# Kernel optimization log

Hardware: AMD Instinct MI355X
Metric: run time of the kernel (lower is better)

## Reference

```python
import jax, jax.numpy as jnp
import numpy as np

HEADS = 8
DIM_HEAD = 64
SCALE = DIM_HEAD ** -0.5


def setup_inputs() -> dict:
    key = jax.random.key(0)
    k1, k2, k3 = jax.random.split(key, 3)
    B, N, D = 4, 2048, HEADS * DIM_HEAD  # D = inner_dim = 512
    x = jax.random.normal(k1, (B, N, D), dtype=jnp.float32)
    # nn.Linear weights stored transposed vs torch; here we use [in, out]
    w_qkv = jax.random.normal(k2, (D, 3 * D), dtype=jnp.float32) * (D ** -0.5)
    w_out = jax.random.normal(k3, (D, D), dtype=jnp.float32) * (D ** -0.5)
    b_out = jnp.zeros((D,), dtype=jnp.float32)
    return {"x": x, "w_qkv": w_qkv, "w_out": w_out, "b_out": b_out}


def reference(x, w_qkv, w_out, b_out):
    B, N, D = x.shape
    qkv = x @ w_qkv  # [B, N, 3D]
    q, k, v = jnp.split(qkv, 3, axis=-1)

    def to_heads(t):  # b n (h d) -> b h n d
        return t.reshape(B, N, HEADS, DIM_HEAD).transpose(0, 2, 1, 3)

    q, k, v = to_heads(q), to_heads(k), to_heads(v)
    dots = jnp.einsum('bhnd,bhmd->bhnm', q, k) * SCALE  # [B,H,N,N]
    attn = jax.nn.softmax(dots, axis=-1)
    out = jnp.einsum('bhnm,bhmd->bhnd', attn, v)  # [B,H,N,d]
    out = out.transpose(0, 2, 1, 3).reshape(B, N, D)  # b h n d -> b n (h d)
    return out @ w_out + b_out
```

## Files before the change

### kernel.cpp

```cpp
#include <hip/hip_runtime.h>

typedef __bf16 bf16;
typedef __bf16 bf16x8 __attribute__((ext_vector_type(8)));
typedef __bf16 bf16x4 __attribute__((ext_vector_type(4)));
typedef float f32x4 __attribute__((ext_vector_type(4)));
typedef float f32x16 __attribute__((ext_vector_type(16)));
typedef unsigned int uint2v __attribute__((ext_vector_type(2)));

#define MFMA16(a, b, c) __builtin_amdgcn_mfma_f32_16x16x32_bf16(a, b, c, 0, 0, 0)
#define MFMA32(a, b, c) __builtin_amdgcn_mfma_f32_32x32x16_bf16(a, b, c, 0, 0, 0)

#define CS 0.18033688011112042f

#if __has_builtin(__builtin_amdgcn_exp2f)
#define EXP2(x) __builtin_amdgcn_exp2f(x)
#else
#define EXP2(x) exp2f(x)
#endif

#define WAIT_VM0() __builtin_amdgcn_s_waitcnt(0x0F70)
#define WAIT_VM6() __builtin_amdgcn_s_waitcnt(0x0F76)
#define WAIT_VM8() __builtin_amdgcn_s_waitcnt(0x0F78)

#define BARRIER() __builtin_amdgcn_s_barrier()
#define CFENCE() asm volatile("" ::: "memory")

__device__ __forceinline__ void load_lds16(const bf16* g, bf16* l) {
    __builtin_amdgcn_global_load_lds(
        (const __attribute__((address_space(1))) unsigned int*)g,
        (__attribute__((address_space(3))) unsigned int*)l, 16, 0, 0);
}

#if __has_builtin(__builtin_amdgcn_permlane32_swap)
__device__ __forceinline__ bf16x8 build_bfrag(bf16x4 plo, bf16x4 phi, int ) {
    union { bf16x4 b; unsigned int i[2]; } ul, uh;
    ul.b = plo; uh.b = phi;
    uint2v r0 = __builtin_amdgcn_permlane32_swap(ul.i[0], uh.i[0], false, false);
    uint2v r1 = __builtin_amdgcn_permlane32_swap(ul.i[1], uh.i[1], false, false);
    union { unsigned int i[4]; bf16x8 b; } ub;
    ub.i[0] = r0[0]; ub.i[1] = r1[0]; ub.i[2] = r0[1]; ub.i[3] = r1[1];
    return ub.b;
}

__device__ __forceinline__ float sum_halves(float x) {
    union { float f; unsigned int u; } a; a.f = x;
    uint2v r = __builtin_amdgcn_permlane32_swap(a.u, a.u, false, false);
    union { unsigned int u; float f; } b0, b1;
    b0.u = r[0]; b1.u = r[1];
    return b0.f + b1.f;
}
#else
__device__ __forceinline__ bf16x4 shfl_xor32_b64(bf16x4 v) {
    union { bf16x4 b; int i[2]; } u;
    u.b = v;
    u.i[0] = __shfl_xor(u.i[0], 32, 64);
    u.i[1] = __shfl_xor(u.i[1], 32, 64);
    return u.b;
}
__device__ __forceinline__ bf16x8 build_bfrag(bf16x4 plo, bf16x4 phi, int h) {
    bf16x4 xlo = shfl_xor32_b64(plo);
    bf16x4 xhi = shfl_xor32_b64(phi);
    bf16x4 lo4 = h ? xhi : plo;
    bf16x4 hi4 = h ? phi : xlo;
    bf16x8 bb;
#pragma unroll
    for (int i = 0; i < 4; ++i) { bb[i] = lo4[i]; bb[4 + i] = hi4[i]; }
    return bb;
}
__device__ __forceinline__ float sum_halves(float x) {
    return x + __shfl_xor(x, 32, 64);
}
#endif

__global__ __launch_bounds__(256) void prep_kernel(const float* __restrict__ x,
                                                   const float* __restrict__ w_qkv,
                                                   const float* __restrict__ w_out,
                                                   bf16* __restrict__ xb,
                                                   bf16* __restrict__ wqkvT,
                                                   bf16* __restrict__ woutT) {
    __shared__ float tile[32][33];
    int bid = blockIdx.x, t = threadIdx.x;
    if (bid < 4096) {
        int i = (bid * 256 + t) * 4;
        float4 v = *(const float4*)&x[i];
        bf16x4 o = {(bf16)v.x, (bf16)v.y, (bf16)v.z, (bf16)v.w};
        *(bf16x4*)&xb[i] = o;
        return;
    }
    const float* in; bf16* out; int C, bx, by;
    if (bid < 4864) { int b2 = bid - 4096; in = w_qkv; out = wqkvT; C = 1536; bx = b2 % 48; by = b2 / 48; }
    else            { int b3 = bid - 4864; in = w_out; out = woutT; C = 512;  bx = b3 & 15; by = b3 >> 4; }
    const int R = 512;
    int tx = t & 31, ty = t >> 5;
    int c0 = bx * 32, r0 = by * 32;
#pragma unroll
    for (int i = ty; i < 32; i += 8)
        tile[i][tx] = in[(size_t)(r0 + i) * C + c0 + tx];
    __syncthreads();
#pragma unroll
    for (int i = ty; i < 32; i += 8)
        out[(size_t)(c0 + i) * R + r0 + tx] = (bf16)tile[tx][i];
}

__global__ __launch_bounds__(256) void transpose_v_kernel(const bf16* __restrict__ qkv,
                                                          bf16* __restrict__ vt) {
    __shared__ bf16 tile[64][68];
    int t = threadIdx.x;
    int bh = blockIdx.z, b = bh >> 3, hd = bh & 7;
    int n0 = blockIdx.x * 64;
    int rr = t >> 4, c4 = (t & 15) * 4;
#pragma unroll
    for (int p = 0; p < 4; ++p) {
        int r = p * 16 + rr;
        *(bf16x4*)&tile[r][c4] =
            *(const bf16x4*)&qkv[(size_t)(b * 2048 + n0 + r) * 1536 + 1024 + hd * 64 + c4];
    }
    __syncthreads();
#pragma unroll
    for (int p = 0; p < 4; ++p) {
        int d = p * 16 + rr;
        bf16x4 o = {tile[c4][d], tile[c4 + 1][d], tile[c4 + 2][d], tile[c4 + 3][d]};
        *(bf16x4*)&vt[(size_t)(bh * 64 + d) * 2048 + n0 + c4] = o;
    }
}

template <int MT, int MODE, typename OutT>
__global__ __launch_bounds__(256, (MT == 4) ? 2 : 3)
void gemm_bt_kernel(const bf16* __restrict__ A,
                    const bf16* __restrict__ Bt,
                    const float* __restrict__ bias,
                    OutT* __restrict__ C,
                    int M, int N, int K) {
    const int BM = MT * 32;
    const int ASZ = BM * 64, BSZ = 128 * 64;
    __shared__ bf16 As[2 * ASZ];
    __shared__ bf16 Bs[2 * BSZ];
    int t = threadIdx.x;
    int lane = t & 63, w = t >> 6;
    int wr = w >> 1, wc = w & 1;
    int quad = lane >> 4, r16 = lane & 15;

    int lin = blockIdx.y * gridDim.x + blockIdx.x;
    int cpx = (gridDim.x * gridDim.y) >> 3;
    int nl = (lin & 7) * cpx + (lin >> 3);
    int bx = nl % gridDim.x, by = nl / gridDim.x;
    int m0 = by * BM, n0 = bx * 128;

    const f32x4 fzero = {0.f, 0.f, 0.f, 0.f};
    f32x4 acc[MT][4];
#pragma unroll
    for (int i = 0; i < MT; ++i)
#pragma unroll
        for (int j = 0; j < 4; ++j) acc[i][j] = fzero;

    const bf16* ap[MT]; bf16* ad[MT];
    const bf16* bp[4];  bf16* bd[4];
#pragma unroll
    for (int i = 0; i < MT; ++i) {
        int ci = i * 256 + t;
        int row = ci >> 3, cp = ci & 7, cc = cp ^ (row & 7);
        ap[i] = &A[(size_t)(m0 + row) * K + cc * 8];
        ad[i] = &As[ci * 8];
    }
#pragma unroll
    for (int i = 0; i < 4; ++i) {
        int ci = i * 256 + t;
        int row = ci >> 3, cp = ci & 7, cc = cp ^ (row & 7);
        bp[i] = &Bt[(size_t)(n0 + row) * K + cc * 8];
        bd[i] = &Bs[ci * 8];
    }

    auto stage = [&](int par) {
#pragma unroll
        for (int i = 0; i < MT; ++i) { load_lds16(ap[i], ad[i] + par * ASZ); ap[i] += 64; }
#pragma unroll
        for (int i = 0; i < 4; ++i) { load_lds16(bp[i], bd[i] + par * BSZ); bp[i] += 64; }
    };

    stage(0);
    int nk = K >> 6;
    for (int kk = 0; kk < nk; ++kk) {
        if (kk + 1 < nk) {
            stage((kk + 1) & 1);
            if constexpr (MT == 4) WAIT_VM8(); else WAIT_VM6();
        } else {
            WAIT_VM0();
        }
        CFENCE(); BARRIER(); CFENCE();

        const bf16* Asb = &As[(kk & 1) * ASZ];
        const bf16* Bsb = &Bs[(kk & 1) * BSZ];
#pragma unroll
        for (int ks = 0; ks < 2; ++ks) {
            bf16x8 af[MT], bfr[4];
            int cp = (ks * 4 + quad) ^ (r16 & 7);
#pragma unroll
            for (int mt = 0; mt < MT; ++mt)
                af[mt] = *(const bf16x8*)&Asb[(wr * (BM / 2) + mt * 16 + r16) * 64 + cp * 8];
#pragma unroll
            for (int nt = 0; nt < 4; ++nt)
                bfr[nt] = *(const bf16x8*)&Bsb[(wc * 64 + nt * 16 + r16) * 64 + cp * 8];
#pragma unroll
            for (int mt = 0; mt < MT; ++mt)
#pragma unroll
                for (int nt = 0; nt < 4; ++nt)
                    acc[mt][nt] = MFMA16(af[mt], bfr[nt], acc[mt][nt]);
        }
        if (kk + 1 < nk) { CFENCE(); BARRIER(); CFENCE(); }
    }
#pragma unroll
    for (int mt = 0; mt < MT; ++mt)
#pragma unroll
        for (int nt = 0; nt < 4; ++nt)
#pragma unroll
            for (int r = 0; r < 4; ++r) {
                int row = m0 + wr * (BM / 2) + mt * 16 + quad * 4 + r;
                int col = n0 + wc * 64 + nt * 16 + r16;
                float v = acc[mt][nt][r];
                if (MODE == 1 && n0 < 512) v *= CS;
                if (MODE == 2) v += bias[col];
                C[(size_t)row * N + col] = (OutT)v;
            }
}

__global__ __launch_bounds__(128, 2) void attn_kernel(const bf16* __restrict__ qkv,
                                                      const bf16* __restrict__ vt,
                                                      bf16* __restrict__ out) {
    __shared__ __align__(16) char smemraw[32768];
    bf16* stage = (bf16*)smemraw;

    int t = threadIdx.x;
    int lane = t & 63, w = t >> 6;
    int h = lane >> 5, q = lane & 31;
    int bh = blockIdx.y, b = bh >> 3, hd = bh & 7;
    int qb = blockIdx.x * 64;

    bf16x8 qf[2][4];
#pragma unroll
    for (int sub = 0; sub < 2; ++sub) {
        size_t qoff = (size_t)(b * 2048 + qb + sub * 32 + q) * 1536 + hd * 64;
#pragma unroll
        for (int s = 0; s < 4; ++s)
            qf[sub][s] = *(const bf16x8*)&qkv[qoff + s * 16 + h * 8];
    }

    f32x16 o_acc[2][2];
#pragma unroll
    for (int sub = 0; sub < 2; ++sub)
#pragma unroll
        for (int db = 0; db < 2; ++db)
#pragma unroll
            for (int i = 0; i < 16; ++i) o_acc[sub][db][i] = 0.f;
    float psum[2] = {0.f, 0.f};

    bf16* base = stage + w * 8192;

    const bf16* kp[4]; const bf16* vp[4];
    int kdo[4], vdo[4];
#pragma unroll
    for (int rdd = 0; rdd < 4; ++rdd) {
        int ciK = rdd * 64 + lane;
        int rowK = ciK >> 3, ccK = (ciK & 7) ^ (rowK & 7);
        kp[rdd] = &qkv[(size_t)(b * 2048 + w * 1024 + rowK) * 1536 + 512 + hd * 64 + ccK * 8];
        kdo[rdd] = ciK * 8;
        int ciV = rdd * 64 + lane;
        int rowV = ciV >> 2, ccV = (ciV & 3) ^ (rowV & 3);
        vp[rdd] = &vt[(size_t)(bh * 64 + rowV) * 2048 + w * 1024 + ccV * 8];
        vdo[rdd] = 2048 + ciV * 8;
    }

#pragma unroll
    for (int rdd = 0; rdd < 4; ++rdd) {
        load_lds16(kp[rdd], base + kdo[rdd]);  kp[rdd] += (size_t)32 * 1536;
        load_lds16(vp[rdd], base + vdo[rdd]);  vp[rdd] += 32;
    }

    for (int it = 0; it < 32; ++it) {
        const bf16* Ks = base + (it & 1) * 4096;
        const bf16* Vs = Ks + 2048;
        if (it < 31) {
            bf16* nb = base + ((it + 1) & 1) * 4096;
#pragma unroll
            for (int rdd = 0; rdd < 4; ++rdd) {
                load_lds16(kp[rdd], nb + kdo[rdd]);  kp[rdd] += (size_t)32 * 1536;
                load_lds16(vp[rdd], nb + vdo[rdd]);  vp[rdd] += 32;
            }
            WAIT_VM8();
        } else {
            WAIT_VM0();
        }

        bf16x8 kf[4];
#pragma unroll
        for (int s = 0; s < 4; ++s) {
            int cp = (s * 2 + h) ^ (q & 7);
            kf[s] = *(const bf16x8*)&Ks[q * 64 + cp * 8];
        }
        bf16x8 vf[2][2];
#pragma unroll
        for (int kstep = 0; kstep < 2; ++kstep)
#pragma unroll
            for (int db = 0; db < 2; ++db) {
                int cp = (kstep * 2 + h) ^ (q & 3);
                vf[kstep][db] = *(const bf16x8*)&Vs[(db * 32 + q) * 32 + cp * 8];
            }

#pragma unroll
        for (int sub = 0; sub < 2; ++sub) {
            f32x16 sacc;
#pragma unroll
            for (int i = 0; i < 16; ++i) sacc[i] = 0.f;
#pragma unroll
            for (int s = 0; s < 4; ++s)
                sacc = MFMA32(kf[s], qf[sub][s], sacc);

            bf16x4 pk[4];
            float ps0 = 0.f, ps1 = 0.f, ps2 = 0.f, ps3 = 0.f;
#pragma unroll
            for (int i = 0; i < 4; ++i) {
                float p0 = EXP2(sacc[i]);
                float p1 = EXP2(sacc[4 + i]);
                float p2 = EXP2(sacc[8 + i]);
                float p3 = EXP2(sacc[12 + i]);
                ps0 += p0; ps1 += p1; ps2 += p2; ps3 += p3;
                pk[0][i] = (bf16)p0; pk[1][i] = (bf16)p1;
                pk[2][i] = (bf16)p2; pk[3][i] = (bf16)p3;
            }
            psum[sub] += (ps0 + ps1) + (ps2 + ps3);
            bf16x8 bfr0 = build_bfrag(pk[0], pk[1], h);
            bf16x8 bfr1 = build_bfrag(pk[2], pk[3], h);

#pragma unroll
            for (int db = 0; db < 2; ++db) {
                o_acc[sub][db] = MFMA32(vf[0][db], bfr0, o_acc[sub][db]);
                o_acc[sub][db] = MFMA32(vf[1][db], bfr1, o_acc[sub][db]);
            }
        }
    }

    float l_own[2];
#pragma unroll
    for (int sub = 0; sub < 2; ++sub)
        l_own[sub] = sum_halves(psum[sub]);

    __syncthreads();
    float* Of = (float*)smemraw;
    float* Lf = (float*)(smemraw + 17408);

    if (w == 1) {
#pragma unroll
        for (int sub = 0; sub < 2; ++sub) {
#pragma unroll
            for (int db = 0; db < 2; ++db)
#pragma unroll
                for (int r = 0; r < 16; ++r) {
                    int d = db * 32 + (r & 3) + 8 * (r >> 2) + 4 * h;
                    Of[(sub * 32 + q) * 68 + d] = o_acc[sub][db][r];
                }
            if (h == 0) Lf[sub * 32 + q] = l_own[sub];
        }
    }
    __syncthreads();
    if (w == 0) {
#pragma unroll
        for (int sub = 0; sub < 2; ++sub) {
#pragma unroll
            for (int db = 0; db < 2; ++db)
#pragma unroll
                for (int r = 0; r < 16; ++r) {
                    int d = db * 32 + (r & 3) + 8 * (r >> 2) + 4 * h;
                    Of[(sub * 32 + q) * 68 + d] += o_acc[sub][db][r];
                }
            if (h == 0) Lf[sub * 32 + q] += l_own[sub];
        }
    }
    __syncthreads();

    {
        int row = t >> 1, half = t & 1;
        float linv = 1.f / Lf[row];
        const float* src = &Of[row * 68 + half * 32];
        bf16* dst = &out[(size_t)(b * 2048 + qb + row) * 512 + hd * 64 + half * 32];
#pragma unroll
        for (int i = 0; i < 4; ++i) {
            f32x4 a = *(const f32x4*)&src[i * 8];
            f32x4 c = *(const f32x4*)&src[i * 8 + 4];
            bf16x8 o8;
#pragma unroll
            for (int j = 0; j < 4; ++j) {
                o8[j] = (bf16)(a[j] * linv);
                o8[4 + j] = (bf16)(c[j] * linv);
            }
            *(bf16x8*)&dst[i * 8] = o8;
        }
    }
}

extern "C" void kernel_launch(void* const* d_in, const int* in_sizes, int n_in,
                              void* d_out, int out_size, void* d_ws, size_t ws_size,
                              hipStream_t stream) {
    const float* x     = (const float*)d_in[0];
    const float* w_qkv = (const float*)d_in[1];
    const float* w_out = (const float*)d_in[2];
    const float* b_out = (const float*)d_in[3];
    float* out = (float*)d_out;

    char* ws = (char*)d_ws;
    size_t off = 0;
    bf16* xb    = (bf16*)(ws + off); off += (size_t)8192 * 512 * 2;
    bf16* wqkvT = (bf16*)(ws + off); off += (size_t)1536 * 512 * 2;
    bf16* woutT = (bf16*)(ws + off); off += (size_t)512 * 512 * 2;
    bf16* qkv   = (bf16*)(ws + off); off += (size_t)8192 * 1536 * 2;
    bf16* vt    = (bf16*)(ws + off); off += (size_t)32 * 64 * 2048 * 2;
    bf16* attn  = (bf16*)(ws + off);

    prep_kernel<<<5120, 256, 0, stream>>>(x, w_qkv, w_out, xb, wqkvT, woutT);
    gemm_bt_kernel<4, 1, bf16><<<dim3(12, 64), 256, 0, stream>>>(
        xb, wqkvT, nullptr, qkv, 8192, 1536, 512);
    transpose_v_kernel<<<dim3(32, 1, 32), 256, 0, stream>>>(qkv, vt);
    attn_kernel<<<dim3(32, 32), 128, 0, stream>>>(qkv, vt, attn);
    gemm_bt_kernel<2, 2, float><<<dim3(4, 128), 256, 0, stream>>>(
        attn, woutT, b_out, out, 8192, 512, 512);
}
```

Measured before the change: 159.6 us.

## Split attention key range across four waves with staggered K/V pipelining

The attention kernel now runs four waves per block instead of two, each covering 512 keys, so the key range is split more finely within a block. Its load pipeline changes to double-buffer K while V uses a single buffer, and QK/softmax for one tile is interleaved with the V load and PV of the previous tile. The cross-wave reduction of partial outputs grows to four serialized LDS accumulation steps. This costs more LDS per block (48KB) and more barriers at the end, in exchange for more waves in flight to hide latency.

```diff
diff --git a/kernel.cpp b/kernel.cpp
--- a/kernel.cpp
+++ b/kernel.cpp
@@ -19,6 +19,7 @@
 #endif
 
 #define WAIT_VM0() __builtin_amdgcn_s_waitcnt(0x0F70)
+#define WAIT_VM4() __builtin_amdgcn_s_waitcnt(0x0F74)
 #define WAIT_VM6() __builtin_amdgcn_s_waitcnt(0x0F76)
 #define WAIT_VM8() __builtin_amdgcn_s_waitcnt(0x0F78)
 
@@ -223,10 +224,10 @@
             }
 }
 
-__global__ __launch_bounds__(128, 2) void attn_kernel(const bf16* __restrict__ qkv,
+__global__ __launch_bounds__(256, 3) void attn_kernel(const bf16* __restrict__ qkv,
                                                       const bf16* __restrict__ vt,
                                                       bf16* __restrict__ out) {
-    __shared__ __align__(16) char smemraw[32768];
+    __shared__ __align__(16) char smemraw[49152];
     bf16* stage = (bf16*)smemraw;
 
     int t = threadIdx.x;
@@ -253,7 +254,8 @@
             for (int i = 0; i < 16; ++i) o_acc[sub][db][i] = 0.f;
     float psum[2] = {0.f, 0.f};
 
-    bf16* base = stage + w * 8192;
+    bf16* base = stage + w * 6144;
+    bf16* Vs = base + 4096;
 
     const bf16* kp[4]; const bf16* vp[4];
     int kdo[4], vdo[4];
@@ -261,59 +263,39 @@
     for (int rdd = 0; rdd < 4; ++rdd) {
         int ciK = rdd * 64 + lane;
         int rowK = ciK >> 3, ccK = (ciK & 7) ^ (rowK & 7);
-        kp[rdd] = &qkv[(size_t)(b * 2048 + w * 1024 + rowK) * 1536 + 512 + hd * 64 + ccK * 8];
+        kp[rdd] = &qkv[(size_t)(b * 2048 + w * 512 + rowK) * 1536 + 512 + hd * 64 + ccK * 8];
         kdo[rdd] = ciK * 8;
         int ciV = rdd * 64 + lane;
         int rowV = ciV >> 2, ccV = (ciV & 3) ^ (rowV & 3);
-        vp[rdd] = &vt[(size_t)(bh * 64 + rowV) * 2048 + w * 1024 + ccV * 8];
-        vdo[rdd] = 2048 + ciV * 8;
-    }
-
-#pragma unroll
-    for (int rdd = 0; rdd < 4; ++rdd) {
-        load_lds16(kp[rdd], base + kdo[rdd]);  kp[rdd] += (size_t)32 * 1536;
-        load_lds16(vp[rdd], base + vdo[rdd]);  vp[rdd] += 32;
-    }
-
-    for (int it = 0; it < 32; ++it) {
-        const bf16* Ks = base + (it & 1) * 4096;
-        const bf16* Vs = Ks + 2048;
-        if (it < 31) {
-            bf16* nb = base + ((it + 1) & 1) * 4096;
-#pragma unroll
-            for (int rdd = 0; rdd < 4; ++rdd) {
-                load_lds16(kp[rdd], nb + kdo[rdd]);  kp[rdd] += (size_t)32 * 1536;
-                load_lds16(vp[rdd], nb + vdo[rdd]);  vp[rdd] += 32;
-            }
-            WAIT_VM8();
-        } else {
-            WAIT_VM0();
-        }
-
-        bf16x8 kf[4];
-#pragma unroll
-        for (int s = 0; s < 4; ++s) {
-            int cp = (s * 2 + h) ^ (q & 7);
-            kf[s] = *(const bf16x8*)&Ks[q * 64 + cp * 8];
-        }
-        bf16x8 vf[2][2];
-#pragma unroll
-        for (int kstep = 0; kstep < 2; ++kstep)
-#pragma unroll
-            for (int db = 0; db < 2; ++db) {
-                int cp = (kstep * 2 + h) ^ (q & 3);
-                vf[kstep][db] = *(const bf16x8*)&Vs[(db * 32 + q) * 32 + cp * 8];
-            }
-
+        vp[rdd] = &vt[(size_t)(bh * 64 + rowV) * 2048 + w * 512 + ccV * 8];
+        vdo[rdd] = ciV * 8;
+    }
+    const size_t KSTEP = (size_t)32 * 1536;
+
+#pragma unroll
+    for (int rdd = 0; rdd < 4; ++rdd) { load_lds16(kp[rdd], base + kdo[rdd]);        kp[rdd] += KSTEP; }
+#pragma unroll
+    for (int rdd = 0; rdd < 4; ++rdd) { load_lds16(vp[rdd], Vs + vdo[rdd]);          vp[rdd] += 32; }
+#pragma unroll
+    for (int rdd = 0; rdd < 4; ++rdd) { load_lds16(kp[rdd], base + 2048 + kdo[rdd]); kp[rdd] += KSTEP; }
+    WAIT_VM8();
+
+    bf16x8 bfr[2][2];
+    auto qk_softmax = [&](const bf16* Ks) {
 #pragma unroll
         for (int sub = 0; sub < 2; ++sub) {
+            bf16x8 kf[4];
+#pragma unroll
+            for (int s = 0; s < 4; ++s) {
+                int cp = (s * 2 + h) ^ (q & 7);
+                kf[s] = *(const bf16x8*)&Ks[q * 64 + cp * 8];
+            }
             f32x16 sacc;
 #pragma unroll
             for (int i = 0; i < 16; ++i) sacc[i] = 0.f;
 #pragma unroll
             for (int s = 0; s < 4; ++s)
                 sacc = MFMA32(kf[s], qf[sub][s], sacc);
-
             bf16x4 pk[4];
             float ps0 = 0.f, ps1 = 0.f, ps2 = 0.f, ps3 = 0.f;
 #pragma unroll
@@ -327,27 +309,59 @@
                 pk[2][i] = (bf16)p2; pk[3][i] = (bf16)p3;
             }
             psum[sub] += (ps0 + ps1) + (ps2 + ps3);
-            bf16x8 bfr0 = build_bfrag(pk[0], pk[1], h);
-            bf16x8 bfr1 = build_bfrag(pk[2], pk[3], h);
-
+            bfr[sub][0] = build_bfrag(pk[0], pk[1], h);
+            bfr[sub][1] = build_bfrag(pk[2], pk[3], h);
+        }
+    };
+    auto pv = [&]() {
+        bf16x8 vf[2][2];
+#pragma unroll
+        for (int kstep = 0; kstep < 2; ++kstep)
 #pragma unroll
             for (int db = 0; db < 2; ++db) {
-                o_acc[sub][db] = MFMA32(vf[0][db], bfr0, o_acc[sub][db]);
-                o_acc[sub][db] = MFMA32(vf[1][db], bfr1, o_acc[sub][db]);
-            }
-        }
-    }
+                int cp = (kstep * 2 + h) ^ (q & 3);
+                vf[kstep][db] = *(const bf16x8*)&Vs[(db * 32 + q) * 32 + cp * 8];
+            }
+#pragma unroll
+        for (int sub = 0; sub < 2; ++sub)
+#pragma unroll
+            for (int db = 0; db < 2; ++db) {
+                o_acc[sub][db] = MFMA32(vf[0][db], bfr[sub][0], o_acc[sub][db]);
+                o_acc[sub][db] = MFMA32(vf[1][db], bfr[sub][1], o_acc[sub][db]);
+            }
+    };
+
+#pragma unroll 1
+    for (int it = 0; it < 14; ++it) {
+        qk_softmax(base + (it & 1) * 2048);
+        WAIT_VM4();
+        pv();
+        CFENCE();
+#pragma unroll
+        for (int rdd = 0; rdd < 4; ++rdd) { load_lds16(vp[rdd], Vs + vdo[rdd]);               vp[rdd] += 32; }
+#pragma unroll
+        for (int rdd = 0; rdd < 4; ++rdd) { load_lds16(kp[rdd], base + (it & 1) * 2048 + kdo[rdd]); kp[rdd] += KSTEP; }
+        WAIT_VM8();
+    }
+    qk_softmax(base);
+    WAIT_VM4();  pv();  CFENCE();
+#pragma unroll
+    for (int rdd = 0; rdd < 4; ++rdd) load_lds16(vp[rdd], Vs + vdo[rdd]);
+    WAIT_VM4();
+    qk_softmax(base + 2048);
+    WAIT_VM0();
+    pv();
 
     float l_own[2];
 #pragma unroll
     for (int sub = 0; sub < 2; ++sub)
         l_own[sub] = sum_halves(psum[sub]);
 
-    __syncthreads();
     float* Of = (float*)smemraw;
     float* Lf = (float*)(smemraw + 17408);
 
-    if (w == 1) {
+    __syncthreads();
+    if (w == 3) {
 #pragma unroll
         for (int sub = 0; sub < 2; ++sub) {
 #pragma unroll
@@ -360,29 +374,32 @@
             if (h == 0) Lf[sub * 32 + q] = l_own[sub];
         }
     }
+#pragma unroll
+    for (int mw = 2; mw >= 0; --mw) {
+        __syncthreads();
+        if (w == mw) {
+#pragma unroll
+            for (int sub = 0; sub < 2; ++sub) {
+#pragma unroll
+                for (int db = 0; db < 2; ++db)
+#pragma unroll
+                    for (int r = 0; r < 16; ++r) {
+                        int d = db * 32 + (r & 3) + 8 * (r >> 2) + 4 * h;
+                        Of[(sub * 32 + q) * 68 + d] += o_acc[sub][db][r];
+                    }
+                if (h == 0) Lf[sub * 32 + q] += l_own[sub];
+            }
+        }
+    }
     __syncthreads();
-    if (w == 0) {
-#pragma unroll
-        for (int sub = 0; sub < 2; ++sub) {
-#pragma unroll
-            for (int db = 0; db < 2; ++db)
-#pragma unroll
-                for (int r = 0; r < 16; ++r) {
-                    int d = db * 32 + (r & 3) + 8 * (r >> 2) + 4 * h;
-                    Of[(sub * 32 + q) * 68 + d] += o_acc[sub][db][r];
-                }
-            if (h == 0) Lf[sub * 32 + q] += l_own[sub];
-        }
-    }
-    __syncthreads();
 
     {
-        int row = t >> 1, half = t & 1;
+        int row = t >> 2, qt = t & 3;
         float linv = 1.f / Lf[row];
-        const float* src = &Of[row * 68 + half * 32];
-        bf16* dst = &out[(size_t)(b * 2048 + qb + row) * 512 + hd * 64 + half * 32];
-#pragma unroll
-        for (int i = 0; i < 4; ++i) {
+        const float* src = &Of[row * 68 + qt * 16];
+        bf16* dst = &out[(size_t)(b * 2048 + qb + row) * 512 + hd * 64 + qt * 16];
+#pragma unroll
+        for (int i = 0; i < 2; ++i) {
             f32x4 a = *(const f32x4*)&src[i * 8];
             f32x4 c = *(const f32x4*)&src[i * 8 + 4];
             bf16x8 o8;
@@ -418,7 +435,7 @@
     gemm_bt_kernel<4, 1, bf16><<<dim3(12, 64), 256, 0, stream>>>(
         xb, wqkvT, nullptr, qkv, 8192, 1536, 512);
     transpose_v_kernel<<<dim3(32, 1, 32), 256, 0, stream>>>(qkv, vt);
-    attn_kernel<<<dim3(32, 32), 128, 0, stream>>>(qkv, vt, attn);
+    attn_kernel<<<dim3(32, 32), 256, 0, stream>>>(qkv, vt, attn);
     gemm_bt_kernel<2, 2, float><<<dim3(4, 128), 256, 0, stream>>>(
         attn, woutT, b_out, out, 8192, 512, 512);
 }
```

Measured after the change: 210.5 us. 1.32x slower.
